# Kernel optimization log

Measured on AMD Instinct MI355X. Metric: run time of the kernel, lower is better.

## Reference

```python
import jax, jax.numpy as jnp
import numpy as np
from jax import lax

ANG = 9
MIND, MAXD = -4, 4
EPS = 1e-5


def conv(x, w, stride=1, dilation=1, padding=0, groups=1):
    return lax.conv_general_dilated(
        x, w, (stride, stride), [(padding, padding)] * 2,
        rhs_dilation=(dilation, dilation),
        dimension_numbers=('NCHW', 'OIHW', 'NCHW'),
        feature_group_count=groups)


def bn_relu(x, g, b):
    # training-mode BatchNorm2d (biased batch stats) + ReLU, as in torch default forward
    m = x.mean((0, 2, 3), keepdims=True)
    v = ((x - m) ** 2).mean((0, 2, 3), keepdims=True)
    y = (x - m) * lax.rsqrt(v + EPS) * g.reshape(1, -1, 1, 1) + b.reshape(1, -1, 1, 1)
    return jax.nn.relu(y)


def sai2macpi(x, ang):
    # out[:, :, i*ang+u, j*ang+v] = x[:, :, u*h+i, v*w+j]  (pure strided rearrange)
    b, c, hu, wv = x.shape
    h, w = hu // ang, wv // ang
    x = x.reshape(b, c, ang, h, ang, w)
    return x.transpose(0, 1, 3, 2, 5, 4).reshape(b, c, h * ang, w * ang)


def _shift_idx(n, ang, dil, pad):
    # per-view-block gather indices replicating Unfold(k=ang,dil,pad,stride=ang)->Fold
    idx = jnp.arange(n)[:, None] * ang + jnp.arange(ang)[None, :] * dil - pad  # [n, ang]
    valid = (idx >= 0) & (idx < n * ang)
    return jnp.clip(idx, 0, n * ang - 1).reshape(-1), valid.reshape(-1)


def disp_shift(feat, d, ang):
    b, c, hu, wv = feat.shape
    h, w = hu // ang, wv // ang
    if d < 0:
        dil = -d * ang + 1
        pad = ang * (ang - 1) * (-d) // 2
    elif d == 0:
        dil, pad = 1, 0
    else:
        dil = d * ang - 1
        pad = ang * (ang - 1) * d // 2 - ang + 1
    ih, mh = _shift_idx(h, ang, dil, pad)
    iw, mw = _shift_idx(w, ang, dil, pad)
    out = feat[:, :, ih, :][:, :, :, iw]
    mask = (mh[:, None] & mw[None, :]).astype(feat.dtype)
    return out * mask


def setup_inputs() -> dict:
    key = jax.random.key(0)
    ks = jax.random.split(key, 16)
    b, h, w = 2, 96, 96
    hu, wv = h * ANG, w * ANG
    s = 0.1
    inp = {
        'x': jax.random.normal(ks[0], (b, 1, hu, wv), jnp.float32),
        'fw0': jax.random.normal(ks[1], (7, 1, 3, 3), jnp.float32) * s,
        'fg0': jnp.ones((7,), jnp.float32),
        'fb0': jnp.zeros((7,), jnp.float32),
        'fw': jax.random.normal(ks[2], (6, 7, 7, 3, 3), jnp.float32) * s,
        'fg': jnp.ones((6, 7), jnp.float32),
        'fb': jnp.zeros((6, 7), jnp.float32),
        'bc_w': jax.random.normal(ks[3], (144, 7, 9, 9), jnp.float32) * 0.04,
        'agg0_dw': jax.random.normal(ks[4], (144, 1, 3, 3), jnp.float32) * s,
        'agg0_dg': jnp.ones((144,), jnp.float32),
        'agg0_db': jnp.zeros((144,), jnp.float32),
        'agg0_pw': jax.random.normal(ks[5], (180, 144, 1, 1), jnp.float32) * s,
        'agg0_pg': jnp.ones((180,), jnp.float32),
        'agg0_pb': jnp.zeros((180,), jnp.float32),
        'aggm_dw': jax.random.normal(ks[6], (4, 180, 1, 3, 3), jnp.float32) * s,
        'aggm_dg': jnp.ones((4, 180), jnp.float32),
        'aggm_db': jnp.zeros((4, 180), jnp.float32),
        'aggm_pw': jax.random.normal(ks[7], (4, 180, 180, 1, 1), jnp.float32) * s,
        'aggm_pg': jnp.ones((4, 180), jnp.float32),
        'aggm_pb': jnp.zeros((4, 180), jnp.float32),
        'last_dw': jax.random.normal(ks[8], (180, 1, 3, 3), jnp.float32) * s,
        'last_dg': jnp.ones((180,), jnp.float32),
        'last_db': jnp.zeros((180,), jnp.float32),
        'last_pw': jax.random.normal(ks[9], (9, 180, 1, 1), jnp.float32) * s,
    }
    return inp


def reference(x, fw0, fg0, fb0, fw, fg, fb, bc_w,
              agg0_dw, agg0_dg, agg0_db, agg0_pw, agg0_pg, agg0_pb,
              aggm_dw, aggm_dg, aggm_db, aggm_pw, aggm_pg, aggm_pb,
              last_dw, last_dg, last_db, last_pw):
    # SAI -> MacPI rearrange
    f = sai2macpi(x, ANG)
    f = bn_relu(conv(f, fw0, dilation=ANG, padding=ANG), fg0, fb0)
    for i in range(6):
        f = bn_relu(conv(f, fw[i], dilation=ANG, padding=ANG), fg[i], fb[i])
    # per-disparity Unfold/Fold shift -> concat [b, 9*7, hu, wv]
    vol = jnp.concatenate([disp_shift(f, d, ANG) for d in range(MIND, MAXD + 1)], axis=1)
    # BuildCost: grouped conv, kernel=stride=angRes -> [b, 144, h, w]
    cv = conv(vol, bc_w, stride=ANG, groups=9)
    # aggregation: depthwise-separable blocks
    y = bn_relu(conv(cv, agg0_dw, padding=1, groups=144), agg0_dg, agg0_db)
    y = bn_relu(conv(y, agg0_pw), agg0_pg, agg0_pb)
    for i in range(4):
        y = bn_relu(conv(y, aggm_dw[i], padding=1, groups=180), aggm_dg[i], aggm_db[i])
        y = bn_relu(conv(y, aggm_pw[i]), aggm_pg[i], aggm_pb[i])
    y = bn_relu(conv(y, last_dw, padding=1, groups=180), last_dg, last_db)
    cost = conv(y, last_pw)  # [b, 9, h, w]
    score = jax.nn.softmax(cost, axis=1)
    disps = jnp.arange(MIND, MAXD + 1, dtype=score.dtype).reshape(1, -1, 1, 1)
    return jnp.sum(score * disps, axis=1, keepdims=True)  # [b, 1, h, w]
```

## Files before the change

kernel.cpp:

```cpp
#include <hip/hip_runtime.h>

#define ANG 9
#define HH 96
#define BB 2
#define PLANE_F (81*HH*HH)
#define PLANE_A (HH*HH)
#define NBLK_FEAT 1458

typedef float f4 __attribute__((ext_vector_type(4), aligned(4)));

__device__ __forceinline__ void row3sel(const float* rp, int base, bool j0, bool j95,
                                        float& w0, float& w1, float& w2) {
  f4 v = *(const f4*)(rp + base);
  w0 = j95 ? v.z : v.x;
  w1 = j0 ? v.x : (j95 ? v.w : v.y);
  w2 = j0 ? v.y : v.z;
}

__global__ __launch_bounds__(256) void k_bnfinal(const float* __restrict__ psum,
    const float* __restrict__ psq, const float* __restrict__ g, const float* __restrict__ bbias,
    float* __restrict__ sc, float* __restrict__ sh, int NB, float invN) {
  int c = blockIdx.x, tid = threadIdx.x;
  float s = 0.f, q = 0.f;
  for (int k = tid; k < NB; k += 256) { s += psum[c * NB + k]; q += psq[c * NB + k]; }
  __shared__ float ss[256], qq[256];
  ss[tid] = s; qq[tid] = q;
  __syncthreads();
  for (int st = 128; st > 0; st >>= 1) {
    if (tid < st) { ss[tid] += ss[tid + st]; qq[tid] += qq[tid + st]; }
    __syncthreads();
  }
  if (tid == 0) {
    float mean = ss[0] * invN;
    float var = fmaxf(qq[0] * invN - mean * mean, 0.f);
    float scale = g[c] / sqrtf(var + 1e-5f);
    sc[c] = scale; sh[c] = bbias[c] - mean * scale;
  }
}

__global__ __launch_bounds__(256) void k_wprep(const float* __restrict__ bcw,
    const float* __restrict__ a0pw, const float* __restrict__ ampw, const float* __restrict__ lpw,
    float* __restrict__ wt, float* __restrict__ wpt) {
  int k = blockIdx.x * 256 + threadIdx.x;
  if (k < 81648) {
    int o = k & 15; int rest = k >> 4;
    int r81 = rest % 81; int gc = rest / 81;
    int c = gc % 7, g = gc / 7;
    wt[k] = bcw[((g * 16 + o) * 7 + c) * 81 + r81];
    return;
  }
  int t = k - 81648;
  if (t < 25920) {
    int c = t / 180, o = t % 180;
    wpt[t] = a0pw[o * 144 + c];
  } else if (t < 25920 + 129600) {
    int t2 = t - 25920;
    int m = t2 / 32400, r = t2 % 32400;
    int c = r / 180, o = r % 180;
    wpt[t] = ampw[m * 32400 + o * 180 + c];
  } else if (t < 25920 + 129600 + 1620) {
    int t2 = t - 25920 - 129600;
    int c = t2 / 9, o = t2 % 9;
    wpt[t] = lpw[o * 180 + c];
  }
}

__global__ __launch_bounds__(256) void k_featconv0(const float* __restrict__ x,
    const float* __restrict__ w, float* __restrict__ out,
    float* __restrict__ psum, float* __restrict__ psq) {
  int blk = blockIdx.x, tid = threadIdx.x;
  int view = blk / 9, q = blk % 9;
  int b = view / 81, uv = view % 81;
  int u = uv / 9, v = uv % 9;
  int widx = q * 256 + tid;
  int j = widx % HH, i0 = (widx / HH) * 4;
  bool j0 = (j == 0), j95 = (j == 95);
  int base = j0 ? 0 : (j95 ? 92 : j - 1);
  float me0 = j0 ? 0.f : 1.f, me2 = j95 ? 0.f : 1.f;
  const float* bx = x + (size_t)b * PLANE_F + (u * HH) * 864 + v * HH;
  float win[6][3];
  #pragma unroll
  for (int r6 = 0; r6 < 6; r6++) {
    int ii = i0 + r6 - 1;
    float mi = ((unsigned)ii < 96u) ? 1.f : 0.f;
    int iic = min(max(ii, 0), 95);
    float w0, w1, w2;
    row3sel(bx + iic * 864, base, j0, j95, w0, w1, w2);
    win[r6][0] = w0 * (mi * me0);
    win[r6][1] = w1 * mi;
    win[r6][2] = w2 * (mi * me2);
  }
  float acc[4][7];
  #pragma unroll
  for (int px = 0; px < 4; px++)
    #pragma unroll
    for (int o = 0; o < 7; o++) acc[px][o] = 0.f;
  #pragma unroll
  for (int o = 0; o < 7; o++) {
    const float* wc = w + o * 9;
    #pragma unroll
    for (int ky = 0; ky < 3; ky++)
      #pragma unroll
      for (int kx = 0; kx < 3; kx++) {
        float wv = wc[ky * 3 + kx];
        #pragma unroll
        for (int px = 0; px < 4; px++)
          acc[px][o] = fmaf(win[px + ky][kx], wv, acc[px][o]);
      }
  }
  #pragma unroll
  for (int o = 0; o < 7; o++) {
    float* op = out + ((size_t)(b * 7 + o)) * PLANE_F + uv * PLANE_A + i0 * HH + j;
    #pragma unroll
    for (int px = 0; px < 4; px++) op[px * HH] = acc[px][o];
  }
  float sv[7], qv[7];
  #pragma unroll
  for (int o = 0; o < 7; o++) {
    sv[o] = acc[0][o] + acc[1][o] + acc[2][o] + acc[3][o];
    qv[o] = acc[0][o]*acc[0][o] + acc[1][o]*acc[1][o] + acc[2][o]*acc[2][o] + acc[3][o]*acc[3][o];
  }
  #pragma unroll
  for (int off2 = 32; off2 > 0; off2 >>= 1)
    #pragma unroll
    for (int o = 0; o < 7; o++) { sv[o] += __shfl_down(sv[o], off2); qv[o] += __shfl_down(qv[o], off2); }
  __shared__ float red[4][14];
  int wave = tid >> 6, lane = tid & 63;
  if (lane == 0) {
    #pragma unroll
    for (int o = 0; o < 7; o++) { red[wave][o] = sv[o]; red[wave][7 + o] = qv[o]; }
  }
  __syncthreads();
  if (tid < 14) {
    float t4 = red[0][tid] + red[1][tid] + red[2][tid] + red[3][tid];
    if (tid < 7) psum[tid * NBLK_FEAT + blk] = t4;
    else         psq[(tid - 7) * NBLK_FEAT + blk] = t4;
  }
}

__global__ __launch_bounds__(256) void k_featconv4(const float* __restrict__ in,
    const float* __restrict__ w, const float* __restrict__ sc, const float* __restrict__ sh,
    float* __restrict__ out, float* __restrict__ psum, float* __restrict__ psq) {
  int blk = blockIdx.x, tid = threadIdx.x;
  int view = blk / 9, q = blk % 9;
  int b = view / 81, uv = view % 81;
  int widx = q * 256 + tid;
  int j = widx % HH, i0 = (widx / HH) * 4;
  bool j0 = (j == 0), j95 = (j == 95);
  int base = j0 ? 0 : (j95 ? 92 : j - 1);
  float me0 = j0 ? 0.f : 1.f, me2 = j95 ? 0.f : 1.f;
  float mrow[6]; int roff[6];
  #pragma unroll
  for (int r6 = 0; r6 < 6; r6++) {
    int ii = i0 + r6 - 1;
    mrow[r6] = ((unsigned)ii < 96u) ? 1.f : 0.f;
    roff[r6] = min(max(ii, 0), 95) * HH + base;
  }
  float acc[4][7];
  #pragma unroll
  for (int px = 0; px < 4; px++)
    #pragma unroll
    for (int o = 0; o < 7; o++) acc[px][o] = 0.f;
  const float* ipbase = in + ((size_t)(b * 7)) * PLANE_F + uv * PLANE_A;
  float pre[6][3];
  #pragma unroll
  for (int r6 = 0; r6 < 6; r6++)
    row3sel(ipbase + roff[r6], 0, j0, j95, pre[r6][0], pre[r6][1], pre[r6][2]);
  #pragma unroll 1
  for (int c = 0; c < 7; c++) {
    float s = sc[c], h2 = sh[c];
    float win[6][3];
    #pragma unroll
    for (int r6 = 0; r6 < 6; r6++) {
      win[r6][0] = fmaxf(fmaf(pre[r6][0], s, h2), 0.f) * (mrow[r6] * me0);
      win[r6][1] = fmaxf(fmaf(pre[r6][1], s, h2), 0.f) * mrow[r6];
      win[r6][2] = fmaxf(fmaf(pre[r6][2], s, h2), 0.f) * (mrow[r6] * me2);
    }
    if (c < 6) {
      const float* ipn = ipbase + (size_t)(c + 1) * PLANE_F;
      #pragma unroll
      for (int r6 = 0; r6 < 6; r6++)
        row3sel(ipn + roff[r6], 0, j0, j95, pre[r6][0], pre[r6][1], pre[r6][2]);
    }
    #pragma unroll
    for (int o = 0; o < 7; o++) {
      const float* wc = w + (o * 7 + c) * 9;
      #pragma unroll
      for (int ky = 0; ky < 3; ky++)
        #pragma unroll
        for (int kx = 0; kx < 3; kx++) {
          float wv = wc[ky * 3 + kx];
          #pragma unroll
          for (int px = 0; px < 4; px++)
            acc[px][o] = fmaf(win[px + ky][kx], wv, acc[px][o]);
        }
    }
  }
  #pragma unroll
  for (int o = 0; o < 7; o++) {
    float* op = out + ((size_t)(b * 7 + o)) * PLANE_F + uv * PLANE_A + i0 * HH + j;
    #pragma unroll
    for (int px = 0; px < 4; px++) op[px * HH] = acc[px][o];
  }
  float sv[7], qv[7];
  #pragma unroll
  for (int o = 0; o < 7; o++) {
    sv[o] = acc[0][o] + acc[1][o] + acc[2][o] + acc[3][o];
    qv[o] = acc[0][o]*acc[0][o] + acc[1][o]*acc[1][o] + acc[2][o]*acc[2][o] + acc[3][o]*acc[3][o];
  }
  #pragma unroll
  for (int off2 = 32; off2 > 0; off2 >>= 1)
    #pragma unroll
    for (int o = 0; o < 7; o++) { sv[o] += __shfl_down(sv[o], off2); qv[o] += __shfl_down(qv[o], off2); }
  __shared__ float red[4][14];
  int wave = tid >> 6, lane = tid & 63;
  if (lane == 0) {
    #pragma unroll
    for (int o = 0; o < 7; o++) { red[wave][o] = sv[o]; red[wave][7 + o] = qv[o]; }
  }
  __syncthreads();
  if (tid < 14) {
    float t4 = red[0][tid] + red[1][tid] + red[2][tid] + red[3][tid];
    if (tid < 7) psum[tid * NBLK_FEAT + blk] = t4;
    else         psq[(tid - 7) * NBLK_FEAT + blk] = t4;
  }
}

__device__ __forceinline__ void bc_load(const float* __restrict__ F, int b, int c, int u,
    int d, int i, int j, float* raw, float* msk) {
  const float* Fc = F + ((size_t)(b * 7 + c)) * PLANE_F + (u * 9) * PLANE_A;
  int ii = i + d * (4 - u);
  float mi = ((unsigned)ii < 96u) ? 1.f : 0.f;
  int iic = min(max(ii, 0), 95);
  const float* Frow = Fc + iic * HH;
  #pragma unroll
  for (int v = 0; v < 9; v++) {
    int jj = j + d * (4 - v);
    float mj = ((unsigned)jj < 96u) ? 1.f : 0.f;
    int jjc = min(max(jj, 0), 95);
    raw[v] = Frow[v * PLANE_A + jjc];
    msk[v] = mi * mj;
  }
}

__global__ __launch_bounds__(256) void k_buildcost(const float* __restrict__ F,
    const float* __restrict__ sc, const float* __restrict__ sh,
    const float* __restrict__ wt, float* __restrict__ cv) {
  int g = blockIdx.x, b = blockIdx.z, tid = threadIdx.x;
  int d = g - 4;
  bool flip = d > 0;
  int p = blockIdx.y * 256 + tid;
  int i = p / HH, j = p % HH;
  float acc[16];
  #pragma unroll
  for (int o = 0; o < 16; o++) acc[o] = 0.f;
  float raw[9], msk[9];
  bc_load(F, b, 0, 0, d, i, j, raw, msk);
  #pragma unroll 1
  for (int cu = 0; cu < 63; cu++) {
    int c = cu / 9, u = cu - c * 9;
    float cr[9], cm[9];
    #pragma unroll
    for (int v = 0; v < 9; v++) { cr[v] = raw[v]; cm[v] = msk[v]; }
    if (cu + 1 < 63) {
      int cn = (cu + 1) / 9, un = (cu + 1) - cn * 9;
      bc_load(F, b, cn, un, d, i, j, raw, msk);
    }
    float s = sc[c], h2 = sh[c];
    int uw = flip ? 8 - u : u;
    const float* wbase = wt + ((size_t)((g * 7 + c) * 81 + uw * 9)) * 16;
    #pragma unroll
    for (int v = 0; v < 9; v++) {
      float a = fmaxf(fmaf(cr[v], s, h2), 0.f) * cm[v];
      int vw = flip ? 8 - v : v;
      const float* wp = wbase + vw * 16;
      #pragma unroll
      for (int o = 0; o < 16; o++) acc[o] = fmaf(wp[o], a, acc[o]);
    }
  }
  size_t cvb = ((size_t)(b * 144 + g * 16)) * PLANE_A + p;
  #pragma unroll
  for (int o = 0; o < 16; o++) cv[cvb + o * PLANE_A] = acc[o];
}

template<bool AFF>
__global__ __launch_bounds__(256) void k_dwconv(const float* __restrict__ in,
    const float* __restrict__ w, const float* __restrict__ isc, const float* __restrict__ ish,
    float* __restrict__ out, float* __restrict__ psum, float* __restrict__ psq, int C) {
  int blk = blockIdx.x, tid = threadIdx.x;
  int q = blk % 9; int rr = blk / 9; int c = rr % C; int b = rr / C;
  int widx = q * 256 + tid;
  int j = widx % HH, i0 = (widx / HH) * 4;
  bool j0 = (j == 0), j95 = (j == 95);
  int base = j0 ? 0 : (j95 ? 92 : j - 1);
  float me0 = j0 ? 0.f : 1.f, me2 = j95 ? 0.f : 1.f;
  float s  = AFF ? isc[c] : 1.f;
  float h2 = AFF ? ish[c] : 0.f;
  const float* wc = w + c * 9;
  const float* ip = in + ((size_t)(b * C + c)) * PLANE_A;
  float win[6][3];
  #pragma unroll
  for (int r6 = 0; r6 < 6; r6++) {
    int ii = i0 + r6 - 1;
    float mi = ((unsigned)ii < 96u) ? 1.f : 0.f;
    int iic = min(max(ii, 0), 95);
    float w0, w1, w2;
    row3sel(ip + iic * HH, base, j0, j95, w0, w1, w2);
    if (AFF) {
      w0 = fmaxf(fmaf(w0, s, h2), 0.f);
      w1 = fmaxf(fmaf(w1, s, h2), 0.f);
      w2 = fmaxf(fmaf(w2, s, h2), 0.f);
    }
    win[r6][0] = w0 * (mi * me0);
    win[r6][1] = w1 * mi;
    win[r6][2] = w2 * (mi * me2);
  }
  float acc[4];
  #pragma unroll
  for (int px = 0; px < 4; px++) acc[px] = 0.f;
  #pragma unroll
  for (int ky = 0; ky < 3; ky++)
    #pragma unroll
    for (int kx = 0; kx < 3; kx++) {
      float wv = wc[ky * 3 + kx];
      #pragma unroll
      for (int px = 0; px < 4; px++)
        acc[px] = fmaf(win[px + ky][kx], wv, acc[px]);
    }
  float* op = out + ((size_t)(b * C + c)) * PLANE_A + i0 * HH + j;
  #pragma unroll
  for (int px = 0; px < 4; px++) op[px * HH] = acc[px];
  float sv = acc[0] + acc[1] + acc[2] + acc[3];
  float qv = acc[0]*acc[0] + acc[1]*acc[1] + acc[2]*acc[2] + acc[3]*acc[3];
  #pragma unroll
  for (int off2 = 32; off2 > 0; off2 >>= 1) { sv += __shfl_down(sv, off2); qv += __shfl_down(qv, off2); }
  __shared__ float red[4][2];
  int wave = tid >> 6, lane = tid & 63;
  if (lane == 0) { red[wave][0] = sv; red[wave][1] = qv; }
  __syncthreads();
  if (tid == 0) {
    float S = red[0][0] + red[1][0] + red[2][0] + red[3][0];
    float Q = red[0][1] + red[1][1] + red[2][1] + red[3][1];
    psum[c * 18 + b * 9 + q] = S;
    psq [c * 18 + b * 9 + q] = Q;
  }
}

template<int K>
__global__ __launch_bounds__(256) void k_pwconv(const float* __restrict__ in,
    const float* __restrict__ sc, const float* __restrict__ sh,
    const float* __restrict__ wpt, float* __restrict__ out,
    float* __restrict__ psum, float* __restrict__ psq) {
  int tid = threadIdx.x;
  int posblk = blockIdx.y;
  int p = posblk * 256 + tid;
  int b = p / PLANE_A, pp = p - b * PLANE_A;
  int obase = blockIdx.x * 18;
  float acc[18];
  #pragma unroll
  for (int o = 0; o < 18; o++) acc[o] = 0.f;
  const float* ib = in + (size_t)b * K * PLANE_A + pp;
  float xn[4];
  #pragma unroll
  for (int q2 = 0; q2 < 4; q2++) xn[q2] = ib[(size_t)q2 * PLANE_A];
  #pragma unroll 1
  for (int c0 = 0; c0 < K; c0 += 4) {
    float xv[4];
    #pragma unroll
    for (int q2 = 0; q2 < 4; q2++) xv[q2] = xn[q2];
    if (c0 + 4 < K) {
      #pragma unroll
      for (int q2 = 0; q2 < 4; q2++) xn[q2] = ib[(size_t)(c0 + 4 + q2) * PLANE_A];
    }
    #pragma unroll
    for (int q2 = 0; q2 < 4; q2++) {
      int c = c0 + q2;
      float v = fmaxf(fmaf(xv[q2], sc[c], sh[c]), 0.f);
      const float* wc = wpt + (size_t)c * 180 + obase;
      #pragma unroll
      for (int o = 0; o < 18; o++)
        acc[o] = fmaf(wc[o], v, acc[o]);
    }
  }
  #pragma unroll
  for (int o = 0; o < 18; o++)
    out[((size_t)(b * 180 + obase + o)) * PLANE_A + pp] = acc[o];
  __shared__ float rs[4][18], rq[4][18];
  int wave = tid >> 6, lane = tid & 63;
  #pragma unroll
  for (int o = 0; o < 18; o++) {
    float s = acc[o], q = acc[o] * acc[o];
    #pragma unroll
    for (int off = 32; off > 0; off >>= 1) { s += __shfl_down(s, off); q += __shfl_down(q, off); }
    if (lane == 0) { rs[wave][o] = s; rq[wave][o] = q; }
  }
  __syncthreads();
  if (tid < 18)
    psum[(obase + tid) * 72 + posblk] = rs[0][tid] + rs[1][tid] + rs[2][tid] + rs[3][tid];
  else if (tid < 36) {
    int o = tid - 18;
    psq[(obase + o) * 72 + posblk] = rq[0][o] + rq[1][o] + rq[2][o] + rq[3][o];
  }
}

__global__ __launch_bounds__(256) void k_final(const float* __restrict__ in,
    const float* __restrict__ sc, const float* __restrict__ sh,
    const float* __restrict__ wpt, float* __restrict__ out) {
  int tid = threadIdx.x;
  int t = blockIdx.x * 256 + tid;
  int b = t / PLANE_A, p = t - b * PLANE_A;
  const float* ib = in + (size_t)b * 180 * PLANE_A + p;
  float acc[9];
  #pragma unroll
  for (int o = 0; o < 9; o++) acc[o] = 0.f;
  float xn[4];
  #pragma unroll
  for (int q2 = 0; q2 < 4; q2++) xn[q2] = ib[(size_t)q2 * PLANE_A];
  #pragma unroll 1
  for (int c0 = 0; c0 < 180; c0 += 4) {
    float xv[4];
    #pragma unroll
    for (int q2 = 0; q2 < 4; q2++) xv[q2] = xn[q2];
    if (c0 + 4 < 180) {
      #pragma unroll
      for (int q2 = 0; q2 < 4; q2++) xn[q2] = ib[(size_t)(c0 + 4 + q2) * PLANE_A];
    }
    #pragma unroll
    for (int q2 = 0; q2 < 4; q2++) {
      int c = c0 + q2;
      float v = fmaxf(fmaf(xv[q2], sc[c], sh[c]), 0.f);
      const float* wc = wpt + (size_t)c * 9;
      #pragma unroll
      for (int o = 0; o < 9; o++) acc[o] = fmaf(wc[o], v, acc[o]);
    }
  }
  float m = acc[0];
  #pragma unroll
  for (int o = 1; o < 9; o++) m = fmaxf(m, acc[o]);
  float se = 0.f, num = 0.f;
  #pragma unroll
  for (int o = 0; o < 9; o++) {
    float e = expf(acc[o] - m);
    se += e;
    num += (float)(o - 4) * e;
  }
  out[t] = num / se;
}

extern "C" void kernel_launch(void* const* d_in, const int* in_sizes, int n_in,
                              void* d_out, int out_size, void* d_ws, size_t ws_size,
                              hipStream_t stream) {
  const float* x    = (const float*)d_in[0];
  const float* fw0  = (const float*)d_in[1];
  const float* fg0  = (const float*)d_in[2];
  const float* fb0  = (const float*)d_in[3];
  const float* fw   = (const float*)d_in[4];
  const float* fg   = (const float*)d_in[5];
  const float* fb   = (const float*)d_in[6];
  const float* bcw  = (const float*)d_in[7];
  const float* a0dw = (const float*)d_in[8];
  const float* a0dg = (const float*)d_in[9];
  const float* a0db = (const float*)d_in[10];
  const float* a0pw = (const float*)d_in[11];
  const float* a0pg = (const float*)d_in[12];
  const float* a0pb = (const float*)d_in[13];
  const float* amdw = (const float*)d_in[14];
  const float* amdg = (const float*)d_in[15];
  const float* amdb = (const float*)d_in[16];
  const float* ampw = (const float*)d_in[17];
  const float* ampg = (const float*)d_in[18];
  const float* ampb = (const float*)d_in[19];
  const float* ldw  = (const float*)d_in[20];
  const float* ldg  = (const float*)d_in[21];
  const float* ldb  = (const float*)d_in[22];
  const float* lpw  = (const float*)d_in[23];
  float* outp = (float*)d_out;

  float* FA    = (float*)d_ws;
  float* FB    = FA + (size_t)BB * 7 * PLANE_F;
  float* CV    = FB + (size_t)BB * 7 * PLANE_F;
  float* GA    = CV + (size_t)BB * 144 * PLANE_A;
  float* GB    = GA + (size_t)BB * 180 * PLANE_A;
  float* PSUM  = GB + (size_t)BB * 180 * PLANE_A;
  float* PSQ   = PSUM + 180 * 288;
  float* SC    = PSQ + 180 * 288;
  float* SH    = SC + 180;
  float* WT    = SH + 180;
  float* WPT   = WT + 81648;
  float* WPT_A0 = WPT;
  float* WPT_AM = WPT + 25920;
  float* WPT_L  = WPT + 25920 + 129600;

  const float invNbig = 1.0f / (float)(BB * PLANE_F);
  const float invNsmall = 1.0f / (float)(BB * PLANE_A);

  k_wprep<<<(238788 + 255) / 256, 256, 0, stream>>>(bcw, a0pw, ampw, lpw, WT, WPT);

  k_featconv0<<<NBLK_FEAT, 256, 0, stream>>>(x, fw0, FA, PSUM, PSQ);
  k_bnfinal<<<7, 256, 0, stream>>>(PSUM, PSQ, fg0, fb0, SC, SH, NBLK_FEAT, invNbig);

  float* cur = FA; float* nxt = FB;
  for (int i = 0; i < 6; i++) {
    k_featconv4<<<NBLK_FEAT, 256, 0, stream>>>(cur, fw + i * 441, SC, SH, nxt, PSUM, PSQ);
    k_bnfinal<<<7, 256, 0, stream>>>(PSUM, PSQ, fg + i * 7, fb + i * 7, SC, SH, NBLK_FEAT, invNbig);
    float* tmp = cur; cur = nxt; nxt = tmp;
  }

  k_buildcost<<<dim3(9, 36, 2), 256, 0, stream>>>(cur, SC, SH, WT, CV);

  k_dwconv<false><<<BB * 144 * 9, 256, 0, stream>>>(CV, a0dw, nullptr, nullptr, GA, PSUM, PSQ, 144);
  k_bnfinal<<<144, 256, 0, stream>>>(PSUM, PSQ, a0dg, a0db, SC, SH, 18, invNsmall);
  k_pwconv<144><<<dim3(10, 72), 256, 0, stream>>>(GA, SC, SH, WPT_A0, GB, PSUM, PSQ);
  k_bnfinal<<<180, 256, 0, stream>>>(PSUM, PSQ, a0pg, a0pb, SC, SH, 72, invNsmall);

  for (int m = 0; m < 4; m++) {
    k_dwconv<true><<<BB * 180 * 9, 256, 0, stream>>>(GB, amdw + m * 1620, SC, SH, GA, PSUM, PSQ, 180);
    k_bnfinal<<<180, 256, 0, stream>>>(PSUM, PSQ, amdg + m * 180, amdb + m * 180, SC, SH, 18, invNsmall);
    k_pwconv<180><<<dim3(10, 72), 256, 0, stream>>>(GA, SC, SH, WPT_AM + m * 32400, GB, PSUM, PSQ);
    k_bnfinal<<<180, 256, 0, stream>>>(PSUM, PSQ, ampg + m * 180, ampb + m * 180, SC, SH, 72, invNsmall);
  }

  k_dwconv<true><<<BB * 180 * 9, 256, 0, stream>>>(GB, ldw, SC, SH, GA, PSUM, PSQ, 180);
  k_bnfinal<<<180, 256, 0, stream>>>(PSUM, PSQ, ldg, ldb, SC, SH, 18, invNsmall);

  k_final<<<72, 256, 0, stream>>>(GA, SC, SH, WPT_L, outp);
}
```

Before: 765.9 us.

## Fold BN finalize into consumer kernels and split buildcost over channel halves

Removes the separate k_bnfinal launches in the aggregation stage. Each dwconv, pwconv and final kernel now reduces the producer's partial sums itself and computes the BN scale and shift in shared memory, using separate partial-sum buffers so producer and consumer do not clash. The buildcost kernel is split across two channel halves that write to separate cost-volume buffers, doubling its grid for more parallelism. The first dwconv sums those two buffers as it loads them. This trades fewer launches and more parallelism for redundant per-block stat reduction and an extra full cost-volume read and write.

New measurement: 704.5 us. 8.0% less time.

```diff
diff --git a/kernel.cpp b/kernel.cpp
--- a/kernel.cpp
+++ b/kernel.cpp
@@ -6,6 +6,7 @@
 #define PLANE_F (81*HH*HH)
 #define PLANE_A (HH*HH)
 #define NBLK_FEAT 1458
+#define INV_NSMALL (1.0f / 18432.0f)
 
 typedef float f4 __attribute__((ext_vector_type(4), aligned(4)));
 
@@ -245,8 +246,11 @@
 
 __global__ __launch_bounds__(256) void k_buildcost(const float* __restrict__ F,
     const float* __restrict__ sc, const float* __restrict__ sh,
-    const float* __restrict__ wt, float* __restrict__ cv) {
-  int g = blockIdx.x, b = blockIdx.z, tid = threadIdx.x;
+    const float* __restrict__ wt, float* __restrict__ cva, float* __restrict__ cvb) {
+  int g = blockIdx.x, tid = threadIdx.x;
+  int b = blockIdx.z >> 1, half = blockIdx.z & 1;
+  int c0 = half ? 4 : 0;
+  int ncu = half ? 27 : 36;
   int d = g - 4;
   bool flip = d > 0;
   int p = blockIdx.y * 256 + tid;
@@ -255,15 +259,15 @@
   #pragma unroll
   for (int o = 0; o < 16; o++) acc[o] = 0.f;
   float raw[9], msk[9];
-  bc_load(F, b, 0, 0, d, i, j, raw, msk);
+  bc_load(F, b, c0, 0, d, i, j, raw, msk);
   #pragma unroll 1
-  for (int cu = 0; cu < 63; cu++) {
-    int c = cu / 9, u = cu - c * 9;
+  for (int cu = 0; cu < ncu; cu++) {
+    int c = c0 + cu / 9, u = cu % 9;
     float cr[9], cm[9];
     #pragma unroll
     for (int v = 0; v < 9; v++) { cr[v] = raw[v]; cm[v] = msk[v]; }
-    if (cu + 1 < 63) {
-      int cn = (cu + 1) / 9, un = (cu + 1) - cn * 9;
+    if (cu + 1 < ncu) {
+      int cn = c0 + (cu + 1) / 9, un = (cu + 1) % 9;
       bc_load(F, b, cn, un, d, i, j, raw, msk);
     }
     float s = sc[c], h2 = sh[c];
@@ -278,26 +282,47 @@
       for (int o = 0; o < 16; o++) acc[o] = fmaf(wp[o], a, acc[o]);
     }
   }
-  size_t cvb = ((size_t)(b * 144 + g * 16)) * PLANE_A + p;
-  #pragma unroll
-  for (int o = 0; o < 16; o++) cv[cvb + o * PLANE_A] = acc[o];
-}
-
-template<bool AFF>
+  float* cv = half ? cvb : cva;
+  size_t cvbase = ((size_t)(b * 144 + g * 16)) * PLANE_A + p;
+  #pragma unroll
+  for (int o = 0; o < 16; o++) cv[cvbase + o * PLANE_A] = acc[o];
+}
+
+template<bool AFF, bool SUM2>
 __global__ __launch_bounds__(256) void k_dwconv(const float* __restrict__ in,
-    const float* __restrict__ w, const float* __restrict__ isc, const float* __restrict__ ish,
-    float* __restrict__ out, float* __restrict__ psum, float* __restrict__ psq, int C) {
+    const float* __restrict__ in2, const float* __restrict__ w,
+    const float* __restrict__ pps, const float* __restrict__ ppq,
+    const float* __restrict__ g, const float* __restrict__ bbias,
+    float* __restrict__ out, float* __restrict__ dps, float* __restrict__ dpq, int C) {
   int blk = blockIdx.x, tid = threadIdx.x;
   int q = blk % 9; int rr = blk / 9; int c = rr % C; int b = rr / C;
+  __shared__ float scsh[2];
+  float s = 1.f, h2 = 0.f;
+  if (AFF) {
+    float si = 0.f, qi = 0.f;
+    if (tid < 64) {
+      si = pps[c * 72 + tid]; qi = ppq[c * 72 + tid];
+      if (tid < 8) { si += pps[c * 72 + 64 + tid]; qi += ppq[c * 72 + 64 + tid]; }
+    }
+    #pragma unroll
+    for (int off = 32; off > 0; off >>= 1) { si += __shfl_down(si, off); qi += __shfl_down(qi, off); }
+    if (tid == 0) {
+      float mean = si * INV_NSMALL;
+      float var = fmaxf(qi * INV_NSMALL - mean * mean, 0.f);
+      float scale = g[c] / sqrtf(var + 1e-5f);
+      scsh[0] = scale; scsh[1] = bbias[c] - mean * scale;
+    }
+    __syncthreads();
+    s = scsh[0]; h2 = scsh[1];
+  }
   int widx = q * 256 + tid;
   int j = widx % HH, i0 = (widx / HH) * 4;
   bool j0 = (j == 0), j95 = (j == 95);
   int base = j0 ? 0 : (j95 ? 92 : j - 1);
   float me0 = j0 ? 0.f : 1.f, me2 = j95 ? 0.f : 1.f;
-  float s  = AFF ? isc[c] : 1.f;
-  float h2 = AFF ? ish[c] : 0.f;
   const float* wc = w + c * 9;
   const float* ip = in + ((size_t)(b * C + c)) * PLANE_A;
+  const float* ip2 = SUM2 ? in2 + ((size_t)(b * C + c)) * PLANE_A : nullptr;
   float win[6][3];
   #pragma unroll
   for (int r6 = 0; r6 < 6; r6++) {
@@ -306,6 +331,11 @@
     int iic = min(max(ii, 0), 95);
     float w0, w1, w2;
     row3sel(ip + iic * HH, base, j0, j95, w0, w1, w2);
+    if (SUM2) {
+      float x0, x1, x2;
+      row3sel(ip2 + iic * HH, base, j0, j95, x0, x1, x2);
+      w0 += x0; w1 += x1; w2 += x2;
+    }
     if (AFF) {
       w0 = fmaxf(fmaf(w0, s, h2), 0.f);
       w1 = fmaxf(fmaf(w1, s, h2), 0.f);
@@ -341,17 +371,29 @@
   if (tid == 0) {
     float S = red[0][0] + red[1][0] + red[2][0] + red[3][0];
     float Q = red[0][1] + red[1][1] + red[2][1] + red[3][1];
-    psum[c * 18 + b * 9 + q] = S;
-    psq [c * 18 + b * 9 + q] = Q;
+    dps[c * 18 + b * 9 + q] = S;
+    dpq[c * 18 + b * 9 + q] = Q;
   }
 }
 
 template<int K>
 __global__ __launch_bounds__(256) void k_pwconv(const float* __restrict__ in,
-    const float* __restrict__ sc, const float* __restrict__ sh,
+    const float* __restrict__ dps, const float* __restrict__ dpq,
+    const float* __restrict__ g, const float* __restrict__ bbias,
     const float* __restrict__ wpt, float* __restrict__ out,
-    float* __restrict__ psum, float* __restrict__ psq) {
+    float* __restrict__ pps, float* __restrict__ ppq) {
   int tid = threadIdx.x;
+  __shared__ float2 scsh[K];
+  if (tid < K) {
+    float S = 0.f, Q = 0.f;
+    #pragma unroll 1
+    for (int k = 0; k < 18; k++) { S += dps[tid * 18 + k]; Q += dpq[tid * 18 + k]; }
+    float mean = S * INV_NSMALL;
+    float var = fmaxf(Q * INV_NSMALL - mean * mean, 0.f);
+    float scale = g[tid] / sqrtf(var + 1e-5f);
+    scsh[tid] = make_float2(scale, bbias[tid] - mean * scale);
+  }
+  __syncthreads();
   int posblk = blockIdx.y;
   int p = posblk * 256 + tid;
   int b = p / PLANE_A, pp = p - b * PLANE_A;
@@ -375,7 +417,8 @@
     #pragma unroll
     for (int q2 = 0; q2 < 4; q2++) {
       int c = c0 + q2;
-      float v = fmaxf(fmaf(xv[q2], sc[c], sh[c]), 0.f);
+      float2 ss = scsh[c];
+      float v = fmaxf(fmaf(xv[q2], ss.x, ss.y), 0.f);
       const float* wc = wpt + (size_t)c * 180 + obase;
       #pragma unroll
       for (int o = 0; o < 18; o++)
@@ -396,17 +439,29 @@
   }
   __syncthreads();
   if (tid < 18)
-    psum[(obase + tid) * 72 + posblk] = rs[0][tid] + rs[1][tid] + rs[2][tid] + rs[3][tid];
+    pps[(obase + tid) * 72 + posblk] = rs[0][tid] + rs[1][tid] + rs[2][tid] + rs[3][tid];
   else if (tid < 36) {
     int o = tid - 18;
-    psq[(obase + o) * 72 + posblk] = rq[0][o] + rq[1][o] + rq[2][o] + rq[3][o];
+    ppq[(obase + o) * 72 + posblk] = rq[0][o] + rq[1][o] + rq[2][o] + rq[3][o];
   }
 }
 
 __global__ __launch_bounds__(256) void k_final(const float* __restrict__ in,
-    const float* __restrict__ sc, const float* __restrict__ sh,
+    const float* __restrict__ dps, const float* __restrict__ dpq,
+    const float* __restrict__ g, const float* __restrict__ bbias,
     const float* __restrict__ wpt, float* __restrict__ out) {
   int tid = threadIdx.x;
+  __shared__ float2 scsh[180];
+  if (tid < 180) {
+    float S = 0.f, Q = 0.f;
+    #pragma unroll 1
+    for (int k = 0; k < 18; k++) { S += dps[tid * 18 + k]; Q += dpq[tid * 18 + k]; }
+    float mean = S * INV_NSMALL;
+    float var = fmaxf(Q * INV_NSMALL - mean * mean, 0.f);
+    float scale = g[tid] / sqrtf(var + 1e-5f);
+    scsh[tid] = make_float2(scale, bbias[tid] - mean * scale);
+  }
+  __syncthreads();
   int t = blockIdx.x * 256 + tid;
   int b = t / PLANE_A, p = t - b * PLANE_A;
   const float* ib = in + (size_t)b * 180 * PLANE_A + p;
@@ -428,7 +483,8 @@
     #pragma unroll
     for (int q2 = 0; q2 < 4; q2++) {
       int c = c0 + q2;
-      float v = fmaxf(fmaf(xv[q2], sc[c], sh[c]), 0.f);
+      float2 ss = scsh[c];
+      float v = fmaxf(fmaf(xv[q2], ss.x, ss.y), 0.f);
       const float* wc = wpt + (size_t)c * 9;
       #pragma unroll
       for (int o = 0; o < 9; o++) acc[o] = fmaf(wc[o], v, acc[o]);
@@ -478,12 +534,15 @@
 
   float* FA    = (float*)d_ws;
   float* FB    = FA + (size_t)BB * 7 * PLANE_F;
-  float* CV    = FB + (size_t)BB * 7 * PLANE_F;
-  float* GA    = CV + (size_t)BB * 144 * PLANE_A;
+  float* CVA   = FB + (size_t)BB * 7 * PLANE_F;
+  float* CVB   = CVA + (size_t)BB * 144 * PLANE_A;
+  float* GA    = CVB + (size_t)BB * 144 * PLANE_A;
   float* GB    = GA + (size_t)BB * 180 * PLANE_A;
   float* PSUM  = GB + (size_t)BB * 180 * PLANE_A;
   float* PSQ   = PSUM + 180 * 288;
-  float* SC    = PSQ + 180 * 288;
+  float* PPS   = PSQ + 180 * 288;
+  float* PPQ   = PPS + 180 * 72;
+  float* SC    = PPQ + 180 * 72;
   float* SH    = SC + 180;
   float* WT    = SH + 180;
   float* WPT   = WT + 81648;
@@ -492,7 +551,6 @@
   float* WPT_L  = WPT + 25920 + 129600;
 
   const float invNbig = 1.0f / (float)(BB * PLANE_F);
-  const float invNsmall = 1.0f / (float)(BB * PLANE_A);
 
   k_wprep<<<(238788 + 255) / 256, 256, 0, stream>>>(bcw, a0pw, ampw, lpw, WT, WPT);
 
@@ -506,22 +564,24 @@
     float* tmp = cur; cur = nxt; nxt = tmp;
   }
 
-  k_buildcost<<<dim3(9, 36, 2), 256, 0, stream>>>(cur, SC, SH, WT, CV);
-
-  k_dwconv<false><<<BB * 144 * 9, 256, 0, stream>>>(CV, a0dw, nullptr, nullptr, GA, PSUM, PSQ, 144);
-  k_bnfinal<<<144, 256, 0, stream>>>(PSUM, PSQ, a0dg, a0db, SC, SH, 18, invNsmall);
-  k_pwconv<144><<<dim3(10, 72), 256, 0, stream>>>(GA, SC, SH, WPT_A0, GB, PSUM, PSQ);
-  k_bnfinal<<<180, 256, 0, stream>>>(PSUM, PSQ, a0pg, a0pb, SC, SH, 72, invNsmall);
+  k_buildcost<<<dim3(9, 36, 4), 256, 0, stream>>>(cur, SC, SH, WT, CVA, CVB);
+
+  k_dwconv<false, true><<<BB * 144 * 9, 256, 0, stream>>>(CVA, CVB, a0dw,
+      nullptr, nullptr, nullptr, nullptr, GA, PSUM, PSQ, 144);
+  k_pwconv<144><<<dim3(10, 72), 256, 0, stream>>>(GA, PSUM, PSQ, a0dg, a0db,
+      WPT_A0, GB, PPS, PPQ);
 
   for (int m = 0; m < 4; m++) {
-    k_dwconv<true><<<BB * 180 * 9, 256, 0, stream>>>(GB, amdw + m * 1620, SC, SH, GA, PSUM, PSQ, 180);
-    k_bnfinal<<<180, 256, 0, stream>>>(PSUM, PSQ, amdg + m * 180, amdb + m * 180, SC, SH, 18, invNsmall);
-    k_pwconv<180><<<dim3(10, 72), 256, 0, stream>>>(GA, SC, SH, WPT_AM + m * 32400, GB, PSUM, PSQ);
-    k_bnfinal<<<180, 256, 0, stream>>>(PSUM, PSQ, ampg + m * 180, ampb + m * 180, SC, SH, 72, invNsmall);
-  }
-
-  k_dwconv<true><<<BB * 180 * 9, 256, 0, stream>>>(GB, ldw, SC, SH, GA, PSUM, PSQ, 180);
-  k_bnfinal<<<180, 256, 0, stream>>>(PSUM, PSQ, ldg, ldb, SC, SH, 18, invNsmall);
-
-  k_final<<<72, 256, 0, stream>>>(GA, SC, SH, WPT_L, outp);
-}
+    const float* pg = (m == 0) ? a0pg : ampg + (m - 1) * 180;
+    const float* pb = (m == 0) ? a0pb : ampb + (m - 1) * 180;
+    k_dwconv<true, false><<<BB * 180 * 9, 256, 0, stream>>>(GB, nullptr, amdw + m * 1620,
+        PPS, PPQ, pg, pb, GA, PSUM, PSQ, 180);
+    k_pwconv<180><<<dim3(10, 72), 256, 0, stream>>>(GA, PSUM, PSQ,
+        amdg + m * 180, amdb + m * 180, WPT_AM + m * 32400, GB, PPS, PPQ);
+  }
+
+  k_dwconv<true, false><<<BB * 180 * 9, 256, 0, stream>>>(GB, nullptr, ldw,
+      PPS, PPQ, ampg + 540, ampb + 540, GA, PSUM, PSQ, 180);
+
+  k_final<<<72, 256, 0, stream>>>(GA, PSUM, PSQ, ldg, ldb, WPT_L, outp);
+}
```
